# Performance work log

Hardware: AMD Instinct MI355X
Metric: run time of the kernel (lower is better)

## Reference

```python
import jax, jax.numpy as jnp
import numpy as np

KE = 14.3996454784255
A0 = 0.52917721092
ZBL_A = (0.1818, 0.5099, 0.2802, 0.02817)
ZBL_B = (3.2, 0.9423, 0.4029, 0.2016)
P = 6
C12 = 1e-4
R_MIN = 0.2
SCALE = 1.0
R12_CUTOFF = 1.5
R12_SWITCH_WIDTH = 0.2

N_NODES = 100_000
N_EDGES = 6_400_000
N_ELEM = 10


def setup_inputs() -> dict:
    key = jax.random.key(0)
    k1, k2, k3 = jax.random.split(key, 3)
    lengths = jax.random.uniform(k1, (N_EDGES,), dtype=jnp.float32) * 5.0
    species = jax.random.randint(k2, (N_NODES,), 0, N_ELEM)
    node_attrs = jax.nn.one_hot(species, N_ELEM, dtype=jnp.float32)
    edge_index = jax.random.randint(k3, (2, N_EDGES), 0, N_NODES)
    atomic_numbers = jnp.array([1, 6, 7, 8, 16, 17, 26, 29, 47, 79], dtype=jnp.float32)
    r_max = jnp.float32(5.0)
    return {"lengths": lengths, "node_attrs": node_attrs, "edge_index": edge_index,
            "atomic_numbers": atomic_numbers, "r_max": r_max}


def _poly_cutoff(r, r_max):
    x = jnp.clip(r / r_max, 0.0, 1.0)
    return (1.0 - x) ** P


def _zbl_edge(r, Zi, Zj, r_max):
    # screening length a = 0.88534 * a0 / (Zi^0.23 + Zj^0.23)
    a = 0.88534 * A0 / (Zi ** 0.23 + Zj ** 0.23)
    x = r / a
    phi = (ZBL_A[0] * jnp.exp(-ZBL_B[0] * x) + ZBL_A[1] * jnp.exp(-ZBL_B[1] * x)
           + ZBL_A[2] * jnp.exp(-ZBL_B[2] * x) + ZBL_A[3] * jnp.exp(-ZBL_B[3] * x))
    V = KE * Zi * Zj * (phi / r) * SCALE
    return V * _poly_cutoff(r, r_max)


def _r12_edge(r, r_max):
    V = C12 / r ** 12
    V = V * _poly_cutoff(r, r_max)
    width = jnp.float32(R12_SWITCH_WIDTH)
    rc = jnp.float32(R12_CUTOFF)
    hard = (r <= rc).astype(r.dtype)
    t = jnp.clip((rc - r) / jnp.maximum(width, 1e-12), 0.0, 1.0)
    smooth = t * t * (3.0 - 2.0 * t)
    cutoff_extra = jnp.where(width > 0, smooth, hard)
    return V * jnp.where(rc > 0, cutoff_extra, jnp.ones_like(r))


def reference(lengths, node_attrs, edge_index, atomic_numbers, r_max):
    n_nodes = node_attrs.shape[0]
    src, dst = edge_index[0], edge_index[1]
    r = jnp.maximum(lengths, R_MIN)
    Z_node = node_attrs @ atomic_numbers  # [N]
    Zi, Zj = Z_node[src], Z_node[dst]
    V_edge = _zbl_edge(r, Zi, Zj, r_max) + _r12_edge(r, r_max)
    # assume_directed_double: V *= 0.5, then half to each endpoint -> 0.25 each
    quarter = 0.25 * V_edge
    node_E = (jax.ops.segment_sum(quarter, src, num_segments=n_nodes)
              + jax.ops.segment_sum(quarter, dst, num_segments=n_nodes))
    return node_E
```

## Files before the change

### kernel.cpp

```cpp
#include <hip/hip_runtime.h>
#include <hip/hip_bf16.h>
#include <stdint.h>


#define KE_CONST 14.3996454784255f
constexpr float INV_AC = 1.0f / (0.88534f * 0.52917721092f);

#define NR 12800
#define NRB 25600
#define PT_MAX 256
#define LDS_SPEC_MAX 147456

#define QSCALE 4096.0f
#define QINV   (1.0f / 4096.0f)

__device__ __forceinline__ float edge_energy_pt(float len, float2 c,
                                                float inv_rmax) {
    float r = fmaxf(len, 0.2f);
    float inv_r = 1.0f / r;

    float u = fmaxf(1.0f - r * inv_rmax, 0.0f);
    float u2 = u * u;
    float pc = u2 * u2 * u2;

    float x = r * c.y;
    float phi = 0.1818f   * __expf(-3.2f    * x)
              + 0.5099f   * __expf(-0.9423f * x)
              + 0.2802f   * __expf(-0.4029f * x)
              + 0.02817f  * __expf(-0.2016f * x);
    float v_zbl = c.x * phi * inv_r * pc;

    float ir2 = inv_r * inv_r;
    float ir4 = ir2 * ir2;
    float ir12 = ir4 * ir4 * ir4;
    float t = fminf(fmaxf((1.5f - r) * 5.0f, 0.0f), 1.0f);
    float sm = t * t * (3.0f - 2.0f * t);
    float v_r12 = 1e-4f * ir12 * pc * sm;

    return 0.25f * (v_zbl + v_r12);
}

__device__ __forceinline__ float edge_energy(float len, float2 zi, float2 zj,
                                             float inv_rmax) {
    float2 c = make_float2(KE_CONST * zi.x * zj.x, (zi.y + zj.y) * INV_AC);
    return edge_energy_pt(len, c, inv_rmax);
}

__device__ __forceinline__ uint16_t f32_to_bf16_rne(float v) {
    uint32_t u = __float_as_uint(v);
    u += 0x7FFFu + ((u >> 16) & 1u);
    return (uint16_t)(u >> 16);
}

__global__ void species_kernel(const float* __restrict__ node_attrs,
                               uint8_t* __restrict__ spec,
                               int n_nodes, int n_elem) {
    int i = blockIdx.x * blockDim.x + threadIdx.x;
    if (i >= n_nodes) return;
    float v = 0.0f;
    for (int k = 0; k < n_elem; ++k)
        v += node_attrs[i * n_elem + k] * (float)k;
    spec[i] = (uint8_t)(v + 0.5f);
}

__global__ void pair_kernel(const float* __restrict__ atomic_numbers,
                            float2* __restrict__ ptab, int n_elem) {
    int idx = threadIdx.x;
    int n2 = n_elem * n_elem;
    if (idx >= n2) return;
    int i = idx / n_elem, j = idx % n_elem;
    float Zi = atomic_numbers[i], Zj = atomic_numbers[j];
    ptab[idx] = make_float2(KE_CONST * Zi * Zj,
                            (powf(Zi, 0.23f) + powf(Zj, 0.23f)) * INV_AC);
}

__global__ void prep_nodes_kernel(const float* __restrict__ node_attrs,
                                  const float* __restrict__ atomic_numbers,
                                  float2* __restrict__ ztab,
                                  int n_nodes, int n_elem) {
    int i = blockIdx.x * blockDim.x + threadIdx.x;
    if (i >= n_nodes) return;
    float z = 0.0f;
    for (int k = 0; k < n_elem; ++k)
        z += node_attrs[i * n_elem + k] * atomic_numbers[k];
    ztab[i] = make_float2(z, powf(z, 0.23f));
}

__global__ __launch_bounds__(1024) void energy_pack_lds_kernel(
    const float* __restrict__ lengths,
    const int* __restrict__ src, const int* __restrict__ dst,
    const uint8_t* __restrict__ spec,
    const float2* __restrict__ ptab_g,
    const float* __restrict__ rmax_ptr,
    unsigned long long* __restrict__ recs,
    int n_edges, int n_nodes, int n_elem, int nb, int qshift, int chunk) {
    extern __shared__ uint8_t lsp[];
    __shared__ float2 pt[PT_MAX];
    int tid = threadIdx.x;

    int n2 = n_elem * n_elem;
    for (int i = tid; i < n2; i += 1024) pt[i] = ptab_g[i];
    {
        int nw = (n_nodes + 3) >> 2;
        const uint32_t* s32 = reinterpret_cast<const uint32_t*>(spec);
        uint32_t* l32 = reinterpret_cast<uint32_t*>(lsp);
        for (int i = tid; i < nw; i += 1024) l32[i] = s32[i];
    }
    __syncthreads();

    const float inv_rmax = 1.0f / rmax_ptr[0];
    const int nb2 = 2 * nb;
    int e0 = blockIdx.x * chunk;
    int e1 = min(e0 + chunk, n_edges);

    for (int base = e0 + tid * 4; base < e1; base += 1024 * 4) {
        if (base + 4 <= e1) {
            float4 L  = *reinterpret_cast<const float4*>(lengths + base);
            int4   S4 = *reinterpret_cast<const int4*>(src + base);
            int4   D4 = *reinterpret_cast<const int4*>(dst + base);
            int sv[4] = {S4.x, S4.y, S4.z, S4.w};
            int dv[4] = {D4.x, D4.y, D4.z, D4.w};
            float lv[4] = {L.x, L.y, L.z, L.w};
            int spi[4], spj[4];
#pragma unroll
            for (int k = 0; k < 4; ++k) {
                spi[k] = lsp[sv[k]];
                spj[k] = lsp[dv[k]];
            }
            unsigned long long rv[4];
#pragma unroll
            for (int k = 0; k < 4; ++k) {
                float2 c = pt[spi[k] * n_elem + spj[k]];
                float q = edge_energy_pt(lv[k], c, inv_rmax);
                uint32_t qu = __float_as_uint(q) >> qshift;
                rv[k] = (unsigned long long)(unsigned)sv[k]
                      | ((unsigned long long)(unsigned)dv[k] << nb)
                      | ((unsigned long long)qu << nb2);
            }
            uint4* outp = reinterpret_cast<uint4*>(recs + base);
            outp[0] = make_uint4((uint32_t)rv[0], (uint32_t)(rv[0] >> 32),
                                 (uint32_t)rv[1], (uint32_t)(rv[1] >> 32));
            outp[1] = make_uint4((uint32_t)rv[2], (uint32_t)(rv[2] >> 32),
                                 (uint32_t)rv[3], (uint32_t)(rv[3] >> 32));
        } else {
            for (int e = base; e < e1; ++e) {
                int si = src[e], di = dst[e];
                float2 c = pt[lsp[si] * n_elem + lsp[di]];
                float q = edge_energy_pt(lengths[e], c, inv_rmax);
                uint32_t qu = __float_as_uint(q) >> qshift;
                recs[e] = (unsigned long long)(unsigned)si
                        | ((unsigned long long)(unsigned)di << nb)
                        | ((unsigned long long)qu << nb2);
            }
        }
    }
}

__global__ __launch_bounds__(256) void energy_pack_kernel(
    const float* __restrict__ lengths,
    const int* __restrict__ src, const int* __restrict__ dst,
    const uint8_t* __restrict__ spec,
    const float2* __restrict__ ptab_g,
    const float* __restrict__ rmax_ptr,
    unsigned long long* __restrict__ recs,
    int n_edges, int total, int n_elem, int nb, int qshift, int vec_ok) {
    __shared__ float2 pt[PT_MAX];
    int tid = threadIdx.x;
    int n2 = n_elem * n_elem;
    for (int i = tid; i < n2; i += 256) pt[i] = ptab_g[i];
    __syncthreads();

    const float inv_rmax = 1.0f / rmax_ptr[0];
    int t = blockIdx.x * blockDim.x + tid;
    int base = t * 4;
    if (base >= total) return;
    int nb2 = 2 * nb;

    if (vec_ok && base + 3 < n_edges) {
        float4 L  = *reinterpret_cast<const float4*>(lengths + base);
        int4   S4 = *reinterpret_cast<const int4*>(src + base);
        int4   D4 = *reinterpret_cast<const int4*>(dst + base);
        int sv[4] = {S4.x, S4.y, S4.z, S4.w};
        int dv[4] = {D4.x, D4.y, D4.z, D4.w};
        float lv[4] = {L.x, L.y, L.z, L.w};
        int spi[4], spj[4];
#pragma unroll
        for (int k = 0; k < 4; ++k) {
            spi[k] = spec[sv[k]];
            spj[k] = spec[dv[k]];
        }
        unsigned long long rv[4];
#pragma unroll
        for (int k = 0; k < 4; ++k) {
            float2 c = pt[spi[k] * n_elem + spj[k]];
            float q = edge_energy_pt(lv[k], c, inv_rmax);
            uint32_t qu = __float_as_uint(q) >> qshift;
            rv[k] = (unsigned long long)(unsigned)sv[k]
                  | ((unsigned long long)(unsigned)dv[k] << nb)
                  | ((unsigned long long)qu << nb2);
        }
        uint4* out = reinterpret_cast<uint4*>(recs + base);
        out[0] = make_uint4((uint32_t)rv[0], (uint32_t)(rv[0] >> 32),
                            (uint32_t)rv[1], (uint32_t)(rv[1] >> 32));
        out[1] = make_uint4((uint32_t)rv[2], (uint32_t)(rv[2] >> 32),
                            (uint32_t)rv[3], (uint32_t)(rv[3] >> 32));
    } else {
        for (int k = 0; k < 4; ++k) {
            int e = base + k;
            if (e >= total) break;
            unsigned long long rec = 0ull;
            if (e < n_edges) {
                int si = src[e], di = dst[e];
                float2 c = pt[spec[si] * n_elem + spec[di]];
                float q = edge_energy_pt(lengths[e], c, inv_rmax);
                uint32_t qu = __float_as_uint(q) >> qshift;
                rec = (unsigned long long)(unsigned)si
                    | ((unsigned long long)(unsigned)di << nb)
                    | ((unsigned long long)qu << (2 * nb));
            }
            recs[e] = rec;
        }
    }
}

__device__ __forceinline__ void accum_rec_i(
    unsigned long long rec, int* __restrict__ acc,
    unsigned base, unsigned nmask, int nb, int nb2, int qshift, unsigned nr) {
    unsigned sn = (unsigned)rec & nmask;
    unsigned dn = (unsigned)(rec >> nb) & nmask;
    float q = __uint_as_float((uint32_t)(rec >> nb2) << qshift);
    int qi = __float2int_rn(q * QSCALE);
    unsigned a = sn - base;
    if (a < nr) atomicAdd(&acc[a], qi);
    unsigned b = dn - base;
    if (b < nr) atomicAdd(&acc[b], qi);
}

__device__ __forceinline__ void accum_rec(
    unsigned long long rec, float* __restrict__ acc,
    unsigned base, unsigned nmask, int nb, int nb2, int qshift, unsigned nr) {
    unsigned sn = (unsigned)rec & nmask;
    unsigned dn = (unsigned)(rec >> nb) & nmask;
    float q = __uint_as_float((uint32_t)(rec >> nb2) << qshift);
    unsigned a = sn - base;
    if (a < nr) atomicAdd(&acc[a], q);
    unsigned b = dn - base;
    if (b < nr) atomicAdd(&acc[b], q);
}

__global__ __launch_bounds__(1024) void accum_big_kernel(
    const unsigned long long* __restrict__ recs,
    uint16_t* __restrict__ partial,
    int n_edges, int S, int EPB, int npad, int nb, int qshift) {
    extern __shared__ int acc[];
    int tid = threadIdx.x;
    const int4 z4 = make_int4(0, 0, 0, 0);
    for (int i = tid * 4; i < NRB; i += 1024 * 4)
        *reinterpret_cast<int4*>(acc + i) = z4;
    __syncthreads();

    int s = blockIdx.x % S;
    int p = blockIdx.x / S;
    const unsigned base = (unsigned)p * NRB;
    const unsigned nmask = (1u << nb) - 1u;
    const int nb2 = 2 * nb;

    int e0 = s * EPB;
    int e1 = min(e0 + EPB, n_edges);

    for (int off = e0 + tid * 8; off < e1; off += 1024 * 8) {
        if (off + 8 <= e1) {
            uint4 r0 = *reinterpret_cast<const uint4*>(recs + off);
            uint4 r1 = *reinterpret_cast<const uint4*>(recs + off + 2);
            uint4 r2 = *reinterpret_cast<const uint4*>(recs + off + 4);
            uint4 r3 = *reinterpret_cast<const uint4*>(recs + off + 6);
            uint4 rr[4] = {r0, r1, r2, r3};
#pragma unroll
            for (int k = 0; k < 4; ++k) {
                unsigned long long ra = (unsigned long long)rr[k].x
                                      | ((unsigned long long)rr[k].y << 32);
                unsigned long long rb = (unsigned long long)rr[k].z
                                      | ((unsigned long long)rr[k].w << 32);
                accum_rec_i(ra, acc, base, nmask, nb, nb2, qshift, NRB);
                accum_rec_i(rb, acc, base, nmask, nb, nb2, qshift, NRB);
            }
        } else {
            for (int e = off; e < e1; ++e)
                accum_rec_i(recs[e], acc, base, nmask, nb, nb2, qshift, NRB);
        }
    }
    __syncthreads();

    uint16_t* __restrict__ row = partial + (size_t)s * npad + base;
    for (int i = tid * 4; i < NRB; i += 1024 * 4) {
        int4 v = *reinterpret_cast<const int4*>(acc + i);
        float f0 = (float)v.x * QINV, f1 = (float)v.y * QINV;
        float f2 = (float)v.z * QINV, f3 = (float)v.w * QINV;
        uint32_t w0 = (uint32_t)f32_to_bf16_rne(f0)
                    | ((uint32_t)f32_to_bf16_rne(f1) << 16);
        uint32_t w1 = (uint32_t)f32_to_bf16_rne(f2)
                    | ((uint32_t)f32_to_bf16_rne(f3) << 16);
        *reinterpret_cast<uint2*>(row + i) = make_uint2(w0, w1);
    }
}

__global__ __launch_bounds__(512) void accum_kernel(
    const unsigned long long* __restrict__ recs,
    uint16_t* __restrict__ partial,
    int n_edges, int S, int EPB, int npad, int nb, int qshift) {
    __shared__ float acc[NR];
    int tid = threadIdx.x;
    for (int i = tid; i < NR; i += 512) acc[i] = 0.0f;
    __syncthreads();

    int s = blockIdx.x % S;
    int p = blockIdx.x / S;
    const unsigned base = (unsigned)p * NR;
    const unsigned nmask = (1u << nb) - 1u;
    const int nb2 = 2 * nb;

    int e0 = s * EPB;
    int e1 = min(e0 + EPB, n_edges);

    for (int off = e0 + tid * 8; off < e1; off += 512 * 8) {
        if (off + 8 <= e1) {
            uint4 r0 = *reinterpret_cast<const uint4*>(recs + off);
            uint4 r1 = *reinterpret_cast<const uint4*>(recs + off + 2);
            uint4 r2 = *reinterpret_cast<const uint4*>(recs + off + 4);
            uint4 r3 = *reinterpret_cast<const uint4*>(recs + off + 6);
            uint4 rr[4] = {r0, r1, r2, r3};
#pragma unroll
            for (int k = 0; k < 4; ++k) {
                unsigned long long ra = (unsigned long long)rr[k].x
                                      | ((unsigned long long)rr[k].y << 32);
                unsigned long long rb = (unsigned long long)rr[k].z
                                      | ((unsigned long long)rr[k].w << 32);
                accum_rec(ra, acc, base, nmask, nb, nb2, qshift, NR);
                accum_rec(rb, acc, base, nmask, nb, nb2, qshift, NR);
            }
        } else {
            for (int e = off; e < e1; ++e)
                accum_rec(recs[e], acc, base, nmask, nb, nb2, qshift, NR);
        }
    }
    __syncthreads();

    uint16_t* __restrict__ row = partial + (size_t)s * npad + base;
    for (int i = tid; i < NR; i += 512)
        row[i] = f32_to_bf16_rne(acc[i]);
}

__global__ void combine_kernel(const uint16_t* __restrict__ partial,
                               float* __restrict__ out,
                               int n_nodes, int S, int npad) {
    int i = blockIdx.x * blockDim.x + threadIdx.x;
    if (i >= n_nodes) return;
    float t = 0.0f;
    for (int s = 0; s < S; ++s) {
        uint32_t h = partial[(size_t)s * npad + i];
        t += __uint_as_float(h << 16);
    }
    out[i] = t;
}

__global__ void zero_out_kernel(float* __restrict__ out, int n) {
    int i = blockIdx.x * blockDim.x + threadIdx.x;
    if (i < n) out[i] = 0.0f;
}

__global__ __launch_bounds__(256) void edge_kernel_atomic(
    const float* __restrict__ lengths,
    const int* __restrict__ src_idx,
    const int* __restrict__ dst_idx,
    const float2* __restrict__ ztab,
    const float* __restrict__ rmax_ptr,
    float* __restrict__ out,
    int n_edges) {
    const float inv_rmax = 1.0f / rmax_ptr[0];
    int t = blockIdx.x * blockDim.x + threadIdx.x;
    int base = t * 4;
    if (base + 3 < n_edges) {
        float4 L = *reinterpret_cast<const float4*>(lengths + base);
        int4 S = *reinterpret_cast<const int4*>(src_idx + base);
        int4 D = *reinterpret_cast<const int4*>(dst_idx + base);
        float l[4] = {L.x, L.y, L.z, L.w};
        int s[4] = {S.x, S.y, S.z, S.w};
        int d[4] = {D.x, D.y, D.z, D.w};
        float2 zs[4], zd[4];
#pragma unroll
        for (int k = 0; k < 4; ++k) { zs[k] = ztab[s[k]]; zd[k] = ztab[d[k]]; }
#pragma unroll
        for (int k = 0; k < 4; ++k) {
            float q = edge_energy(l[k], zs[k], zd[k], inv_rmax);
            unsafeAtomicAdd(&out[s[k]], q);
            unsafeAtomicAdd(&out[d[k]], q);
        }
    } else if (base < n_edges) {
        for (int e = base; e < n_edges; ++e) {
            int si = src_idx[e], di = dst_idx[e];
            float q = edge_energy(lengths[e], ztab[si], ztab[di], inv_rmax);
            unsafeAtomicAdd(&out[si], q);
            unsafeAtomicAdd(&out[di], q);
        }
    }
}

extern "C" void kernel_launch(void* const* d_in, const int* in_sizes, int n_in,
                              void* d_out, int out_size, void* d_ws, size_t ws_size,
                              hipStream_t stream) {
    const float* lengths        = (const float*)d_in[0];
    const float* node_attrs     = (const float*)d_in[1];
    const int*   edge_index     = (const int*)d_in[2];
    const float* atomic_numbers = (const float*)d_in[3];
    const float* rmax_ptr       = (const float*)d_in[4];

    int n_edges = in_sizes[0];
    int n_elem  = in_sizes[3];
    int n_nodes = out_size;
    float* out = (float*)d_out;

    const int* src = edge_index;
    const int* dst = edge_index + n_edges;

    int vec_ok = ((n_edges & 3) == 0) ? 1 : 0;

    int nb = 1;
    while ((1u << nb) < (unsigned)n_nodes) nb++;
    int qb = 64 - 2 * nb;
    if (qb > 32) qb = 32;
    int qshift = 32 - qb;
    bool pack_ok = (2 * nb + 16 <= 64) && (n_elem * n_elem <= PT_MAX);

    int nb_nodes = (n_nodes + 255) / 256;
    int spec_bytes = (n_nodes + 3) & ~3;

    static int big_ok = -1;
    if (big_ok < 0) {
        big_ok = (hipFuncSetAttribute(
                      reinterpret_cast<const void*>(accum_big_kernel),
                      hipFuncAttributeMaxDynamicSharedMemorySize,
                      NRB * 4) == hipSuccess) ? 1 : 0;
    }
    static int pack_lds_ok = -1;
    if (pack_lds_ok < 0) {
        pack_lds_ok = (hipFuncSetAttribute(
                           reinterpret_cast<const void*>(energy_pack_lds_kernel),
                           hipFuncAttributeMaxDynamicSharedMemorySize,
                           LDS_SPEC_MAX) == hipSuccess) ? 1 : 0;
    }
    bool use_lds_pack = pack_lds_ok && (spec_bytes <= LDS_SPEC_MAX);

    if (pack_ok && big_ok) {
        int P    = (n_nodes + NRB - 1) / NRB;
        int npad = P * NRB;
        int S = (256 / P) & ~7;
        if (S < 8) S = 8;
        size_t part_off = 0, ptab_off = 0, spec_off = 0, need = 0;
        int EPB = 0, TOTAL = 0;
        for (; S >= 8; S -= 8) {
            EPB = (((n_edges + S - 1) / S) + 4095) & ~4095;
            TOTAL = S * EPB;
            part_off = ((size_t)TOTAL * 8 + 255) & ~(size_t)255;
            ptab_off = (part_off + (size_t)S * npad * 2 + 255) & ~(size_t)255;
            spec_off = (ptab_off + (size_t)n_elem * n_elem * 8 + 255) & ~(size_t)255;
            need     = spec_off + (size_t)spec_bytes;
            if (need <= ws_size) break;
        }
        if (S >= 8) {
            unsigned long long* recs = (unsigned long long*)d_ws;
            uint16_t* partial = (uint16_t*)((char*)d_ws + part_off);
            float2*   ptab    = (float2*)((char*)d_ws + ptab_off);
            uint8_t*  spec    = (uint8_t*)((char*)d_ws + spec_off);

            species_kernel<<<nb_nodes, 256, 0, stream>>>(
                node_attrs, spec, n_nodes, n_elem);
            pair_kernel<<<1, PT_MAX, 0, stream>>>(atomic_numbers, ptab, n_elem);
            if (use_lds_pack) {
                int chunk = (((n_edges + 255) / 256) + 3) & ~3;
                energy_pack_lds_kernel<<<256, 1024, spec_bytes, stream>>>(
                    lengths, src, dst, spec, ptab, rmax_ptr, recs,
                    n_edges, n_nodes, n_elem, nb, qshift, chunk);
            } else {
                int nb_energy = TOTAL / 1024;
                energy_pack_kernel<<<nb_energy, 256, 0, stream>>>(
                    lengths, src, dst, spec, ptab, rmax_ptr, recs,
                    n_edges, TOTAL, n_elem, nb, qshift, vec_ok);
            }
            accum_big_kernel<<<P * S, 1024, NRB * 4, stream>>>(
                recs, partial, n_edges, S, EPB, npad, nb, qshift);
            combine_kernel<<<nb_nodes, 256, 0, stream>>>(
                partial, out, n_nodes, S, npad);
            return;
        }
    }

    if (pack_ok) {
        int P    = (n_nodes + NR - 1) / NR;
        int npad = P * NR;
        int S = (768 / P) & ~7;
        if (S < 8) S = 8;
        size_t part_off = 0, ptab_off = 0, spec_off = 0, need = 0;
        int EPB = 0, TOTAL = 0;
        for (; S >= 8; S -= 8) {
            EPB = (((n_edges + S - 1) / S) + 4095) & ~4095;
            TOTAL = S * EPB;
            part_off = ((size_t)TOTAL * 8 + 255) & ~(size_t)255;
            ptab_off = (part_off + (size_t)S * npad * 2 + 255) & ~(size_t)255;
            spec_off = (ptab_off + (size_t)n_elem * n_elem * 8 + 255) & ~(size_t)255;
            need     = spec_off + (size_t)spec_bytes;
            if (need <= ws_size) break;
        }
        if (S >= 8) {
            unsigned long long* recs = (unsigned long long*)d_ws;
            uint16_t* partial = (uint16_t*)((char*)d_ws + part_off);
            float2*   ptab    = (float2*)((char*)d_ws + ptab_off);
            uint8_t*  spec    = (uint8_t*)((char*)d_ws + spec_off);

            species_kernel<<<nb_nodes, 256, 0, stream>>>(
                node_attrs, spec, n_nodes, n_elem);
            pair_kernel<<<1, PT_MAX, 0, stream>>>(atomic_numbers, ptab, n_elem);
            int nb_energy = TOTAL / 1024;
            energy_pack_kernel<<<nb_energy, 256, 0, stream>>>(
                lengths, src, dst, spec, ptab, rmax_ptr, recs,
                n_edges, TOTAL, n_elem, nb, qshift, vec_ok);
            accum_kernel<<<P * S, 512, 0, stream>>>(
                recs, partial, n_edges, S, EPB, npad, nb, qshift);
            combine_kernel<<<nb_nodes, 256, 0, stream>>>(
                partial, out, n_nodes, S, npad);
            return;
        }
    }

    {
        int stride = ((n_nodes + 49) / 2) * 2;
        int R = 16;
        while (R > 1 &&
               (size_t)R * stride * sizeof(float) + (size_t)n_nodes * sizeof(float2)
                   > ws_size)
            R >>= 1;
        float2* ztab = (float2*)((char*)d_ws + (size_t)R * stride * sizeof(float));
        hipMemsetAsync(d_ws, 0, (size_t)R * stride * sizeof(float), stream);
        prep_nodes_kernel<<<nb_nodes, 256, 0, stream>>>(
            node_attrs, atomic_numbers, ztab, n_nodes, n_elem);
        zero_out_kernel<<<nb_nodes, 256, 0, stream>>>(out, n_nodes);
        int n_thread4 = (n_edges + 3) / 4;
        int nb_edges = (n_thread4 + 255) / 256;
        edge_kernel_atomic<<<nb_edges, 256, 0, stream>>>(
            lengths, src, dst, ztab, rmax_ptr, out, n_edges);
    }
}
```

Measured before the change: 164.2 us.

## Store per-edge energy as fp16 and re-read indices in accumulation

Replaces the 64-bit packed (src,dst,q) edge records with a 2-byte fp16 energy array, and has the accumulation kernel re-read src/dst from the inputs. The LDS bin width grows to 32768 nodes per partition. This cuts the intermediate write traffic at the cost of more index reads per partition pass and reduced energy precision (fp16 range/rounding).

```diff
diff --git a/kernel.cpp b/kernel.cpp
--- a/kernel.cpp
+++ b/kernel.cpp
@@ -1,5 +1,6 @@
 #include <hip/hip_runtime.h>
 #include <hip/hip_bf16.h>
+#include <hip/hip_fp16.h>
 #include <stdint.h>
 
 
@@ -7,7 +8,7 @@
 constexpr float INV_AC = 1.0f / (0.88534f * 0.52917721092f);
 
 #define NR 12800
-#define NRB 25600
+#define NRQ 32768
 #define PT_MAX 256
 #define LDS_SPEC_MAX 147456
 
@@ -86,14 +87,14 @@
     ztab[i] = make_float2(z, powf(z, 0.23f));
 }
 
-__global__ __launch_bounds__(1024) void energy_pack_lds_kernel(
+__global__ __launch_bounds__(1024) void energy_q_lds_kernel(
     const float* __restrict__ lengths,
     const int* __restrict__ src, const int* __restrict__ dst,
     const uint8_t* __restrict__ spec,
     const float2* __restrict__ ptab_g,
     const float* __restrict__ rmax_ptr,
-    unsigned long long* __restrict__ recs,
-    int n_edges, int n_nodes, int n_elem, int nb, int qshift, int chunk) {
+    __half* __restrict__ qout,
+    int n_edges, int n_nodes, int n_elem, int chunk) {
     extern __shared__ uint8_t lsp[];
     __shared__ float2 pt[PT_MAX];
     int tid = threadIdx.x;
@@ -109,7 +110,6 @@
     __syncthreads();
 
     const float inv_rmax = 1.0f / rmax_ptr[0];
-    const int nb2 = 2 * nb;
     int e0 = blockIdx.x * chunk;
     int e1 = min(e0 + chunk, n_edges);
 
@@ -127,32 +127,87 @@
                 spi[k] = lsp[sv[k]];
                 spj[k] = lsp[dv[k]];
             }
-            unsigned long long rv[4];
+            float q[4];
 #pragma unroll
             for (int k = 0; k < 4; ++k) {
                 float2 c = pt[spi[k] * n_elem + spj[k]];
-                float q = edge_energy_pt(lv[k], c, inv_rmax);
-                uint32_t qu = __float_as_uint(q) >> qshift;
-                rv[k] = (unsigned long long)(unsigned)sv[k]
-                      | ((unsigned long long)(unsigned)dv[k] << nb)
-                      | ((unsigned long long)qu << nb2);
-            }
-            uint4* outp = reinterpret_cast<uint4*>(recs + base);
-            outp[0] = make_uint4((uint32_t)rv[0], (uint32_t)(rv[0] >> 32),
-                                 (uint32_t)rv[1], (uint32_t)(rv[1] >> 32));
-            outp[1] = make_uint4((uint32_t)rv[2], (uint32_t)(rv[2] >> 32),
-                                 (uint32_t)rv[3], (uint32_t)(rv[3] >> 32));
+                q[k] = edge_energy_pt(lv[k], c, inv_rmax);
+            }
+            __half2 h01 = __floats2half2_rn(q[0], q[1]);
+            __half2 h23 = __floats2half2_rn(q[2], q[3]);
+            uint32_t w0, w1;
+            memcpy(&w0, &h01, 4);
+            memcpy(&w1, &h23, 4);
+            *reinterpret_cast<uint2*>(qout + base) = make_uint2(w0, w1);
         } else {
             for (int e = base; e < e1; ++e) {
                 int si = src[e], di = dst[e];
                 float2 c = pt[lsp[si] * n_elem + lsp[di]];
-                float q = edge_energy_pt(lengths[e], c, inv_rmax);
-                uint32_t qu = __float_as_uint(q) >> qshift;
-                recs[e] = (unsigned long long)(unsigned)si
-                        | ((unsigned long long)(unsigned)di << nb)
-                        | ((unsigned long long)qu << nb2);
-            }
-        }
+                qout[e] = __float2half_rn(edge_energy_pt(lengths[e], c, inv_rmax));
+            }
+        }
+    }
+}
+
+__global__ __launch_bounds__(1024) void accum_q_kernel(
+    const int* __restrict__ src, const int* __restrict__ dst,
+    const __half* __restrict__ qv,
+    uint16_t* __restrict__ partial,
+    int n_edges, int S, int EPB, int npad) {
+    extern __shared__ int acc[];
+    int tid = threadIdx.x;
+    const int4 z4 = make_int4(0, 0, 0, 0);
+    for (int i = tid * 4; i < NRQ; i += 1024 * 4)
+        *reinterpret_cast<int4*>(acc + i) = z4;
+    __syncthreads();
+
+    int s = blockIdx.x % S;
+    int p = blockIdx.x / S;
+    const unsigned base = (unsigned)p * NRQ;
+
+    int e0 = s * EPB;
+    int e1 = min(e0 + EPB, n_edges);
+
+    for (int off = e0 + tid * 4; off < e1; off += 1024 * 4) {
+        if (off + 4 <= e1) {
+            int4 S4 = *reinterpret_cast<const int4*>(src + off);
+            int4 D4 = *reinterpret_cast<const int4*>(dst + off);
+            __half2 h01 = *reinterpret_cast<const __half2*>(qv + off);
+            __half2 h23 = *reinterpret_cast<const __half2*>(qv + off + 2);
+            float qf[4] = {__low2float(h01), __high2float(h01),
+                           __low2float(h23), __high2float(h23)};
+            int sv[4] = {S4.x, S4.y, S4.z, S4.w};
+            int dv[4] = {D4.x, D4.y, D4.z, D4.w};
+#pragma unroll
+            for (int k = 0; k < 4; ++k) {
+                int qi = __float2int_rn(qf[k] * QSCALE);
+                unsigned a = (unsigned)sv[k] - base;
+                if (a < NRQ) atomicAdd(&acc[a], qi);
+                unsigned b = (unsigned)dv[k] - base;
+                if (b < NRQ) atomicAdd(&acc[b], qi);
+            }
+        } else {
+            for (int e = off; e < e1; ++e) {
+                int qi = __float2int_rn(__half2float(qv[e]) * QSCALE);
+                unsigned a = (unsigned)src[e] - base;
+                if (a < NRQ) atomicAdd(&acc[a], qi);
+                unsigned b = (unsigned)dst[e] - base;
+                if (b < NRQ) atomicAdd(&acc[b], qi);
+            }
+        }
+    }
+    __syncthreads();
+
+    uint16_t* __restrict__ row = partial + (size_t)s * npad + base;
+    for (int i = tid * 4; i < NRQ; i += 1024 * 4) {
+        int4 v = *reinterpret_cast<const int4*>(acc + i);
+        float f0 = (float)v.x * QINV, f1 = (float)v.y * QINV;
+        float f2 = (float)v.z * QINV, f3 = (float)v.w * QINV;
+        uint32_t w0 = (uint32_t)f32_to_bf16_rne(f0)
+                    | ((uint32_t)f32_to_bf16_rne(f1) << 16);
+        uint32_t w1 = (uint32_t)f32_to_bf16_rne(f2)
+                    | ((uint32_t)f32_to_bf16_rne(f3) << 16);
+        *reinterpret_cast<uint2*>(row + i) = make_uint2(w0, w1);
     }
 }
 
@@ -223,19 +278,6 @@
     }
 }
 
-__device__ __forceinline__ void accum_rec_i(
-    unsigned long long rec, int* __restrict__ acc,
-    unsigned base, unsigned nmask, int nb, int nb2, int qshift, unsigned nr) {
-    unsigned sn = (unsigned)rec & nmask;
-    unsigned dn = (unsigned)(rec >> nb) & nmask;
-    float q = __uint_as_float((uint32_t)(rec >> nb2) << qshift);
-    int qi = __float2int_rn(q * QSCALE);
-    unsigned a = sn - base;
-    if (a < nr) atomicAdd(&acc[a], qi);
-    unsigned b = dn - base;
-    if (b < nr) atomicAdd(&acc[b], qi);
-}
-
 __device__ __forceinline__ void accum_rec(
     unsigned long long rec, float* __restrict__ acc,
     unsigned base, unsigned nmask, int nb, int nb2, int qshift, unsigned nr) {
@@ -246,62 +288,6 @@
     if (a < nr) atomicAdd(&acc[a], q);
     unsigned b = dn - base;
     if (b < nr) atomicAdd(&acc[b], q);
-}
-
-__global__ __launch_bounds__(1024) void accum_big_kernel(
-    const unsigned long long* __restrict__ recs,
-    uint16_t* __restrict__ partial,
-    int n_edges, int S, int EPB, int npad, int nb, int qshift) {
-    extern __shared__ int acc[];
-    int tid = threadIdx.x;
-    const int4 z4 = make_int4(0, 0, 0, 0);
-    for (int i = tid * 4; i < NRB; i += 1024 * 4)
-        *reinterpret_cast<int4*>(acc + i) = z4;
-    __syncthreads();
-
-    int s = blockIdx.x % S;
-    int p = blockIdx.x / S;
-    const unsigned base = (unsigned)p * NRB;
-    const unsigned nmask = (1u << nb) - 1u;
-    const int nb2 = 2 * nb;
-
-    int e0 = s * EPB;
-    int e1 = min(e0 + EPB, n_edges);
-
-    for (int off = e0 + tid * 8; off < e1; off += 1024 * 8) {
-        if (off + 8 <= e1) {
-            uint4 r0 = *reinterpret_cast<const uint4*>(recs + off);
-            uint4 r1 = *reinterpret_cast<const uint4*>(recs + off + 2);
-            uint4 r2 = *reinterpret_cast<const uint4*>(recs + off + 4);
-            uint4 r3 = *reinterpret_cast<const uint4*>(recs + off + 6);
-            uint4 rr[4] = {r0, r1, r2, r3};
-#pragma unroll
-            for (int k = 0; k < 4; ++k) {
-                unsigned long long ra = (unsigned long long)rr[k].x
-                                      | ((unsigned long long)rr[k].y << 32);
-                unsigned long long rb = (unsigned long long)rr[k].z
-                                      | ((unsigned long long)rr[k].w << 32);
-                accum_rec_i(ra, acc, base, nmask, nb, nb2, qshift, NRB);
-                accum_rec_i(rb, acc, base, nmask, nb, nb2, qshift, NRB);
-            }
-        } else {
-            for (int e = off; e < e1; ++e)
-                accum_rec_i(recs[e], acc, base, nmask, nb, nb2, qshift, NRB);
-        }
-    }
-    __syncthreads();
-
-    uint16_t* __restrict__ row = partial + (size_t)s * npad + base;
-    for (int i = tid * 4; i < NRB; i += 1024 * 4) {
-        int4 v = *reinterpret_cast<const int4*>(acc + i);
-        float f0 = (float)v.x * QINV, f1 = (float)v.y * QINV;
-        float f2 = (float)v.z * QINV, f3 = (float)v.w * QINV;
-        uint32_t w0 = (uint32_t)f32_to_bf16_rne(f0)
-                    | ((uint32_t)f32_to_bf16_rne(f1) << 16);
-        uint32_t w1 = (uint32_t)f32_to_bf16_rne(f2)
-                    | ((uint32_t)f32_to_bf16_rne(f3) << 16);
-        *reinterpret_cast<uint2*>(row + i) = make_uint2(w0, w1);
-    }
 }
 
 __global__ __launch_bounds__(512) void accum_kernel(
@@ -424,50 +410,43 @@
 
     int vec_ok = ((n_edges & 3) == 0) ? 1 : 0;
 
-    int nb = 1;
-    while ((1u << nb) < (unsigned)n_nodes) nb++;
-    int qb = 64 - 2 * nb;
-    if (qb > 32) qb = 32;
-    int qshift = 32 - qb;
-    bool pack_ok = (2 * nb + 16 <= 64) && (n_elem * n_elem <= PT_MAX);
-
     int nb_nodes = (n_nodes + 255) / 256;
     int spec_bytes = (n_nodes + 3) & ~3;
 
-    static int big_ok = -1;
-    if (big_ok < 0) {
-        big_ok = (hipFuncSetAttribute(
-                      reinterpret_cast<const void*>(accum_big_kernel),
-                      hipFuncAttributeMaxDynamicSharedMemorySize,
-                      NRB * 4) == hipSuccess) ? 1 : 0;
+    static int accq_ok = -1;
+    if (accq_ok < 0) {
+        accq_ok = (hipFuncSetAttribute(
+                       reinterpret_cast<const void*>(accum_q_kernel),
+                       hipFuncAttributeMaxDynamicSharedMemorySize,
+                       NRQ * 4) == hipSuccess) ? 1 : 0;
     }
     static int pack_lds_ok = -1;
     if (pack_lds_ok < 0) {
         pack_lds_ok = (hipFuncSetAttribute(
-                           reinterpret_cast<const void*>(energy_pack_lds_kernel),
+                           reinterpret_cast<const void*>(energy_q_lds_kernel),
                            hipFuncAttributeMaxDynamicSharedMemorySize,
                            LDS_SPEC_MAX) == hipSuccess) ? 1 : 0;
     }
-    bool use_lds_pack = pack_lds_ok && (spec_bytes <= LDS_SPEC_MAX);
-
-    if (pack_ok && big_ok) {
-        int P    = (n_nodes + NRB - 1) / NRB;
-        int npad = P * NRB;
+
+    if (accq_ok && pack_lds_ok && (spec_bytes <= LDS_SPEC_MAX)
+        && (n_elem * n_elem <= PT_MAX)) {
+        int P    = (n_nodes + NRQ - 1) / NRQ;
+        int npad = P * NRQ;
         int S = (256 / P) & ~7;
         if (S < 8) S = 8;
         size_t part_off = 0, ptab_off = 0, spec_off = 0, need = 0;
-        int EPB = 0, TOTAL = 0;
+        int EPB = 0;
         for (; S >= 8; S -= 8) {
             EPB = (((n_edges + S - 1) / S) + 4095) & ~4095;
-            TOTAL = S * EPB;
-            part_off = ((size_t)TOTAL * 8 + 255) & ~(size_t)255;
+            size_t q_bytes = ((size_t)n_edges * 2 + 255) & ~(size_t)255;
+            part_off = q_bytes;
             ptab_off = (part_off + (size_t)S * npad * 2 + 255) & ~(size_t)255;
             spec_off = (ptab_off + (size_t)n_elem * n_elem * 8 + 255) & ~(size_t)255;
             need     = spec_off + (size_t)spec_bytes;
             if (need <= ws_size) break;
         }
         if (S >= 8) {
-            unsigned long long* recs = (unsigned long long*)d_ws;
+            __half*   qarr    = (__half*)d_ws;
             uint16_t* partial = (uint16_t*)((char*)d_ws + part_off);
             float2*   ptab    = (float2*)((char*)d_ws + ptab_off);
             uint8_t*  spec    = (uint8_t*)((char*)d_ws + spec_off);
@@ -475,59 +454,61 @@
             species_kernel<<<nb_nodes, 256, 0, stream>>>(
                 node_attrs, spec, n_nodes, n_elem);
             pair_kernel<<<1, PT_MAX, 0, stream>>>(atomic_numbers, ptab, n_elem);
-            if (use_lds_pack) {
-                int chunk = (((n_edges + 255) / 256) + 3) & ~3;
-                energy_pack_lds_kernel<<<256, 1024, spec_bytes, stream>>>(
-                    lengths, src, dst, spec, ptab, rmax_ptr, recs,
-                    n_edges, n_nodes, n_elem, nb, qshift, chunk);
-            } else {
+            int chunk = (((n_edges + 255) / 256) + 3) & ~3;
+            energy_q_lds_kernel<<<256, 1024, spec_bytes, stream>>>(
+                lengths, src, dst, spec, ptab, rmax_ptr, qarr,
+                n_edges, n_nodes, n_elem, chunk);
+            accum_q_kernel<<<P * S, 1024, NRQ * 4, stream>>>(
+                src, dst, qarr, partial, n_edges, S, EPB, npad);
+            combine_kernel<<<nb_nodes, 256, 0, stream>>>(
+                partial, out, n_nodes, S, npad);
+            return;
+        }
+    }
+
+    {
+        int nb = 1;
+        while ((1u << nb) < (unsigned)n_nodes) nb++;
+        int qb = 64 - 2 * nb;
+        if (qb > 32) qb = 32;
+        int qshift = 32 - qb;
+        bool pack_ok = (2 * nb + 16 <= 64) && (n_elem * n_elem <= PT_MAX);
+
+        if (pack_ok) {
+            int P    = (n_nodes + NR - 1) / NR;
+            int npad = P * NR;
+            int S = (768 / P) & ~7;
+            if (S < 8) S = 8;
+            size_t part_off = 0, ptab_off = 0, spec_off = 0, need = 0;
+            int EPB = 0, TOTAL = 0;
+            for (; S >= 8; S -= 8) {
+                EPB = (((n_edges + S - 1) / S) + 4095) & ~4095;
+                TOTAL = S * EPB;
+                part_off = ((size_t)TOTAL * 8 + 255) & ~(size_t)255;
+                ptab_off = (part_off + (size_t)S * npad * 2 + 255) & ~(size_t)255;
+                spec_off = (ptab_off + (size_t)n_elem * n_elem * 8 + 255) & ~(size_t)255;
+                need     = spec_off + (size_t)spec_bytes;
+                if (need <= ws_size) break;
+            }
+            if (S >= 8) {
+                unsigned long long* recs = (unsigned long long*)d_ws;
+                uint16_t* partial = (uint16_t*)((char*)d_ws + part_off);
+                float2*   ptab    = (float2*)((char*)d_ws + ptab_off);
+                uint8_t*  spec    = (uint8_t*)((char*)d_ws + spec_off);
+
+                species_kernel<<<nb_nodes, 256, 0, stream>>>(
+                    node_attrs, spec, n_nodes, n_elem);
+                pair_kernel<<<1, PT_MAX, 0, stream>>>(atomic_numbers, ptab, n_elem);
                 int nb_energy = TOTAL / 1024;
                 energy_pack_kernel<<<nb_energy, 256, 0, stream>>>(
                     lengths, src, dst, spec, ptab, rmax_ptr, recs,
                     n_edges, TOTAL, n_elem, nb, qshift, vec_ok);
-            }
-            accum_big_kernel<<<P * S, 1024, NRB * 4, stream>>>(
-                recs, partial, n_edges, S, EPB, npad, nb, qshift);
-            combine_kernel<<<nb_nodes, 256, 0, stream>>>(
-                partial, out, n_nodes, S, npad);
-            return;
-        }
-    }
-
-    if (pack_ok) {
-        int P    = (n_nodes + NR - 1) / NR;
-        int npad = P * NR;
-        int S = (768 / P) & ~7;
-        if (S < 8) S = 8;
-        size_t part_off = 0, ptab_off = 0, spec_off = 0, need = 0;
-        int EPB = 0, TOTAL = 0;
-        for (; S >= 8; S -= 8) {
-            EPB = (((n_edges + S - 1) / S) + 4095) & ~4095;
-            TOTAL = S * EPB;
-            part_off = ((size_t)TOTAL * 8 + 255) & ~(size_t)255;
-            ptab_off = (part_off + (size_t)S * npad * 2 + 255) & ~(size_t)255;
-            spec_off = (ptab_off + (size_t)n_elem * n_elem * 8 + 255) & ~(size_t)255;
-            need     = spec_off + (size_t)spec_bytes;
-            if (need <= ws_size) break;
-        }
-        if (S >= 8) {
-            unsigned long long* recs = (unsigned long long*)d_ws;
-            uint16_t* partial = (uint16_t*)((char*)d_ws + part_off);
-            float2*   ptab    = (float2*)((char*)d_ws + ptab_off);
-            uint8_t*  spec    = (uint8_t*)((char*)d_ws + spec_off);
-
-            species_kernel<<<nb_nodes, 256, 0, stream>>>(
-                node_attrs, spec, n_nodes, n_elem);
-            pair_kernel<<<1, PT_MAX, 0, stream>>>(atomic_numbers, ptab, n_elem);
-            int nb_energy = TOTAL / 1024;
-            energy_pack_kernel<<<nb_energy, 256, 0, stream>>>(
-                lengths, src, dst, spec, ptab, rmax_ptr, recs,
-                n_edges, TOTAL, n_elem, nb, qshift, vec_ok);
-            accum_kernel<<<P * S, 512, 0, stream>>>(
-                recs, partial, n_edges, S, EPB, npad, nb, qshift);
-            combine_kernel<<<nb_nodes, 256, 0, stream>>>(
-                partial, out, n_nodes, S, npad);
-            return;
+                accum_kernel<<<P * S, 512, 0, stream>>>(
+                    recs, partial, n_edges, S, EPB, npad, nb, qshift);
+                combine_kernel<<<nb_nodes, 256, 0, stream>>>(
+                    partial, out, n_nodes, S, npad);
+                return;
+            }
         }
     }
 
```

New measurement: 154.1 us. -6.2%, faster.
